# Kernel tuning notes

Measured on AMD Instinct MI355X. Metric: run time of the kernel, lower is better.

Reference implementation:

```python
import jax, jax.numpy as jnp
import numpy as np

D_MODEL, D_CTX, D_HEAD = 1024, 768, 16

def setup_inputs() -> dict:
    key = jax.random.key(0)
    ks = jax.random.split(key, 10)
    B, M, N = 8, 4096, 4096
    s = lambda d: 1.0 / np.sqrt(d)
    return {
        "x": jax.random.normal(ks[0], (B, M, D_MODEL), dtype=jnp.float32),
        "context": jax.random.normal(ks[1], (B, N, D_CTX), dtype=jnp.float32),
        "Wq": jax.random.uniform(ks[2], (D_MODEL, D_HEAD), jnp.float32, -s(D_MODEL), s(D_MODEL)),
        "bq": jax.random.uniform(ks[3], (D_HEAD,), jnp.float32, -s(D_MODEL), s(D_MODEL)),
        "Wk": jax.random.uniform(ks[4], (D_CTX, D_HEAD), jnp.float32, -s(D_CTX), s(D_CTX)),
        "bk": jax.random.uniform(ks[5], (D_HEAD,), jnp.float32, -s(D_CTX), s(D_CTX)),
        "Wv": jax.random.uniform(ks[6], (D_CTX, D_HEAD), jnp.float32, -s(D_CTX), s(D_CTX)),
        "bv": jax.random.uniform(ks[7], (D_HEAD,), jnp.float32, -s(D_CTX), s(D_CTX)),
        "Wo": jax.random.uniform(ks[8], (D_HEAD, D_MODEL), jnp.float32, -s(D_HEAD), s(D_HEAD)),
        "bo": jax.random.uniform(ks[9], (D_MODEL,), jnp.float32, -s(D_HEAD), s(D_HEAD)),
    }

def _kernel(t):
    # ELU+1 feature map (non-negative)
    return jax.nn.elu(t) + 1.0

def reference(x, context, Wq, bq, Wk, bk, Wv, bv, Wo, bo):
    Q = _kernel(x @ Wq + bq)            # (B, M, d_head)
    K = _kernel(context @ Wk + bk)      # (B, N, d_head)
    V = context @ Wv + bv               # (B, N, d_head)
    KtV = jnp.einsum('bnd,bne->bde', K, V)   # (B, d_head, d_head)
    num = jnp.einsum('bmd,bde->bme', Q, KtV) # (B, M, d_head)
    K_sum = K.sum(axis=1)                    # (B, d_head)
    denom = jnp.einsum('bmd,bd->bm', Q, K_sum)[..., None] + 1e-6
    out = num / denom                        # (B, M, d_head)
    return out @ Wo + bo                     # (B, M, d_model)
```

## Files before the change

kernel.cpp:

```cpp
#include <hip/hip_runtime.h>
#include <math.h>

#define B_   8
#define M_   4096
#define N_   4096
#define DM   1024
#define DC   768
#define DH   16
#define PD   8
#define KVBLOCKS (B_*N_/32)
#define QBLOCKS  (B_*M_/32)

typedef float v4f __attribute__((ext_vector_type(4)));
typedef __attribute__((ext_vector_type(8))) short short8v;
typedef __attribute__((ext_vector_type(4))) float f32x4;
typedef __attribute__((ext_vector_type(4))) int int4v;

__device__ __forceinline__ float elu1(float t) {
    return t > 0.0f ? t + 1.0f : expf(t);
}
__device__ __forceinline__ float4 ld4(const float* p) { return *reinterpret_cast<const float4*>(p); }
__device__ __forceinline__ void  st4(float* p, float4 v) { *reinterpret_cast<float4*>(p) = v; }
__device__ __forceinline__ void  st4nt(float* p, float4 v) {
    v4f w; w.x = v.x; w.y = v.y; w.z = v.z; w.w = v.w;
    __builtin_nontemporal_store(w, reinterpret_cast<v4f*>(p));
}
__device__ __forceinline__ void fma4(float4& a, float s, float4 w) {
    a.x = fmaf(s, w.x, a.x); a.y = fmaf(s, w.y, a.y);
    a.z = fmaf(s, w.z, a.z); a.w = fmaf(s, w.w, a.w);
}
__device__ __forceinline__ short f2bf(float f) {
    unsigned u = __float_as_uint(f);
    unsigned r = 0x7FFFu + ((u >> 16) & 1u);
    return (short)((u + r) >> 16);
}
__device__ __forceinline__ unsigned cvtpk(float a, float b) {
    unsigned r;
    asm("v_cvt_pk_bf16_f32 %0, %1, %2" : "=v"(r) : "v"(a), "v"(b));
    return r;
}
__device__ __forceinline__ short8v mk_frag(const float4& a, const float4& b) {
    int4v iv;
    iv.x = (int)cvtpk(a.x, a.y);
    iv.y = (int)cvtpk(a.z, a.w);
    iv.z = (int)cvtpk(b.x, b.y);
    iv.w = (int)cvtpk(b.z, b.w);
    union { int4v i; short8v s; } u; u.i = iv;
    return u.s;
}

__global__ __launch_bounds__(256) void prep(
    const float* __restrict__ Wq, const float* __restrict__ Wk,
    const float* __restrict__ Wv,
    short* __restrict__ fq, short* __restrict__ fk, short* __restrict__ fv)
{
    const int id = blockIdx.x * 256 + threadIdx.x;
    if (id >= 80 * 64) return;
    const int l  = id & 63;
    const int kt = id >> 6;
    const float* W; short* dst; int ktl;
    if (kt < 32)      { W = Wq; dst = fq; ktl = kt; }
    else if (kt < 56) { W = Wk; dst = fk; ktl = kt - 32; }
    else              { W = Wv; dst = fv; ktl = kt - 56; }
    const int k0 = ktl * 32 + (l >> 4) * 8;
    const int d  = l & 15;
    short* o = dst + ((size_t)ktl * 64 + l) * 8;
    #pragma unroll
    for (int j = 0; j < 8; ++j)
        o[j] = f2bf(W[(size_t)(k0 + j) * DH + d]);
}

__global__ __launch_bounds__(256) void kvr(
    const float* __restrict__ ctx,
    const short* __restrict__ fk, const short* __restrict__ fv,
    const float* __restrict__ bk, const float* __restrict__ bv,
    float* __restrict__ comb)
{
    __shared__ struct {
        float ka[2][2][16][17];
        float va[2][2][16][17];
        float sk[32][17];
        float sv[32][17];
    } sh;

    const int t  = threadIdx.x;
    const int l  = t & 63;
    const int w  = t >> 6;
    const int rt = w & 1;
    const int kh = w >> 1;
    const int g4 = l >> 4;
    const int lr = l & 15;

    float4 pa[PD], pb[PD];
    const size_t row0 = (size_t)blockIdx.x * 32;
    const float* src = ctx + (row0 + rt*16 + lr) * DC + kh*384 + g4*8;
    f32x4 accK = {0,0,0,0}, accV = {0,0,0,0};

    #pragma unroll
    for (int i = 0; i < PD; ++i) {
        pa[i] = ld4(src + i*32);
        pb[i] = ld4(src + i*32 + 4);
    }
    #pragma unroll
    for (int kt = 0; kt < 12; ++kt) {
        const int st = kt & (PD-1);
        const short8v a = mk_frag(pa[st], pb[st]);
        if (kt + PD < 12) {
            pa[st] = ld4(src + (kt+PD)*32);
            pb[st] = ld4(src + (kt+PD)*32 + 4);
        }
        const int ktg = kh*12 + kt;
        const short8v bkf = *reinterpret_cast<const short8v*>(fk + ((size_t)ktg*64 + l)*8);
        const short8v bvf = *reinterpret_cast<const short8v*>(fv + ((size_t)ktg*64 + l)*8);
        accK = __builtin_amdgcn_mfma_f32_16x16x32_bf16(a, bkf, accK, 0, 0, 0);
        accV = __builtin_amdgcn_mfma_f32_16x16x32_bf16(a, bvf, accV, 0, 0, 0);
    }

    #pragma unroll
    for (int j = 0; j < 4; ++j) {
        sh.ka[rt][kh][g4*4 + j][lr] = accK[j];
        sh.va[rt][kh][g4*4 + j][lr] = accV[j];
    }
    __syncthreads();

    #pragma unroll
    for (int i = t; i < 512; i += 256) {
        const int r = i >> 4, c = i & 15;
        const int rr = r >> 4, wr = r & 15;
        const float kk = sh.ka[rr][0][wr][c] + sh.ka[rr][1][wr][c] + bk[c];
        const float vv = sh.va[rr][0][wr][c] + sh.va[rr][1][wr][c] + bv[c];
        sh.sk[r][c] = elu1(kk);
        sh.sv[r][c] = vv;
    }
    __syncthreads();

    const int d = t >> 4, e = t & 15;
    float acc = 0.f;
    #pragma unroll 16
    for (int n = 0; n < 32; ++n) acc += sh.sk[n][d] * sh.sv[n][e];
    float* p = comb + (size_t)(blockIdx.x >> 7) * 272;
    atomicAdd(&p[t], acc);
    if (t < DH) {
        float ss = 0.f;
        #pragma unroll 16
        for (int n = 0; n < 32; ++n) ss += sh.sk[n][t];
        atomicAdd(&p[256 + t], ss);
    }
}

__global__ __launch_bounds__(256) void qproj(
    const float* __restrict__ x,
    const short* __restrict__ fq, const float* __restrict__ bq,
    const float* __restrict__ comb,
    const float* __restrict__ Wo, const float* __restrict__ bo,
    float* __restrict__ out)
{
    __shared__ float qa[2][2][16][17];
    __shared__ float ql[32 * DH];
    __shared__ float ol[32 * DH];
    __shared__ float kts[272];

    const int t  = threadIdx.x;
    const int l  = t & 63;
    const int w  = t >> 6;
    const int rt = w & 1;
    const int kh = w >> 1;
    const int g4 = l >> 4;
    const int lr = l & 15;
    const size_t row0 = (size_t)blockIdx.x * 32;
    const int b = blockIdx.x >> 7;

    const float* src = x + (row0 + rt*16 + lr) * DM + kh*512 + g4*8;
    float4 pa[PD], pb[PD];
    #pragma unroll
    for (int i = 0; i < PD; ++i) {
        pa[i] = ld4(src + i*32);
        pb[i] = ld4(src + i*32 + 4);
    }
    if (t < 68) st4(&kts[t*4], ld4(comb + (size_t)b*272 + t*4));

    f32x4 accQ = {0,0,0,0};
    #pragma unroll
    for (int kt = 0; kt < 16; ++kt) {
        const int st = kt & (PD-1);
        const short8v a = mk_frag(pa[st], pb[st]);
        if (kt + PD < 16) {
            pa[st] = ld4(src + (kt+PD)*32);
            pb[st] = ld4(src + (kt+PD)*32 + 4);
        }
        const int ktg = kh*16 + kt;
        const short8v bqf = *reinterpret_cast<const short8v*>(fq + ((size_t)ktg*64 + l)*8);
        accQ = __builtin_amdgcn_mfma_f32_16x16x32_bf16(a, bqf, accQ, 0, 0, 0);
    }
    #pragma unroll
    for (int j = 0; j < 4; ++j)
        qa[rt][kh][g4*4 + j][lr] = accQ[j];
    __syncthreads();

    #pragma unroll
    for (int i = t; i < 512; i += 256) {
        const int r = i >> 4, c = i & 15;
        const int rr = r >> 4, wr = r & 15;
        const float v = qa[rr][0][wr][c] + qa[rr][1][wr][c] + bq[c];
        ql[r*DH + c] = elu1(v);
    }
    __syncthreads();

    if (t < 128) {
        const float* qrow = &ql[(t >> 2) * DH];
        const int jj = (t & 3) * 4;
        float den = 1e-6f;
        float4 num = make_float4(0,0,0,0);
        #pragma unroll
        for (int d4 = 0; d4 < 4; ++d4) {
            const float4 q4  = ld4(&qrow[d4*4]);
            const float4 ks4 = ld4(&kts[256 + d4*4]);
            den += q4.x*ks4.x + q4.y*ks4.y + q4.z*ks4.z + q4.w*ks4.w;
            fma4(num, q4.x, ld4(&kts[(d4*4+0)*DH + jj]));
            fma4(num, q4.y, ld4(&kts[(d4*4+1)*DH + jj]));
            fma4(num, q4.z, ld4(&kts[(d4*4+2)*DH + jj]));
            fma4(num, q4.w, ld4(&kts[(d4*4+3)*DH + jj]));
        }
        const float inv = 1.0f / den;
        float4 o4; o4.x = num.x*inv; o4.y = num.y*inv; o4.z = num.z*inv; o4.w = num.w*inv;
        st4(&ol[(t >> 2)*DH + jj], o4);
    }
    __syncthreads();

    float4 wreg[16];
    #pragma unroll
    for (int e = 0; e < 16; ++e) wreg[e] = ld4(Wo + (size_t)e*DM + t*4);
    const float4 bov = ld4(bo + t*4);

    #pragma unroll 4
    for (int r = 0; r < 32; ++r) {
        float4 a = bov;
        #pragma unroll
        for (int eo = 0; eo < 4; ++eo) {
            const float4 o4 = ld4(&ol[r*DH + eo*4]);
            fma4(a, o4.x, wreg[eo*4+0]); fma4(a, o4.y, wreg[eo*4+1]);
            fma4(a, o4.z, wreg[eo*4+2]); fma4(a, o4.w, wreg[eo*4+3]);
        }
        st4nt(out + (row0 + r)*DM + t*4, a);
    }
}

extern "C" void kernel_launch(void* const* d_in, const int* in_sizes, int n_in,
                              void* d_out, int out_size, void* d_ws, size_t ws_size,
                              hipStream_t stream) {
    const float* x    = (const float*)d_in[0];
    const float* ctx  = (const float*)d_in[1];
    const float* Wq   = (const float*)d_in[2];
    const float* bq   = (const float*)d_in[3];
    const float* Wk   = (const float*)d_in[4];
    const float* bk   = (const float*)d_in[5];
    const float* Wv   = (const float*)d_in[6];
    const float* bv   = (const float*)d_in[7];
    const float* Wo   = (const float*)d_in[8];
    const float* bo   = (const float*)d_in[9];
    float* out = (float*)d_out;

    float* ws = (float*)d_ws;
    float* comb = ws;
    short* fq = (short*)(comb + (size_t)B_*272);
    short* fk = fq + (size_t)32*64*8;
    short* fv = fk + (size_t)24*64*8;

    hipMemsetAsync(comb, 0, (size_t)B_*272*sizeof(float), stream);
    prep<<<dim3(20), dim3(256), 0, stream>>>(Wq, Wk, Wv, fq, fk, fv);
    kvr<<<dim3(KVBLOCKS), dim3(256), 0, stream>>>(ctx, fk, fv, bk, bv, comb);
    qproj<<<dim3(QBLOCKS), dim3(256), 0, stream>>>(x, fq, bq, comb, Wo, bo, out);
}
```

Baseline: 74.72 us.

## Replace float atomics with per-block partials and last-block reduction

Each kvr block now writes its 272-float partial (KtV and K_sum) to a workspace slot instead of atomically adding into the per-batch accumulator. A per-batch counter, zeroed in prep, picks the last-finishing block, which sums the 128 partials into comb. This removes the hipMemsetAsync launch and the contention on 272 float atomics per batch from 128 blocks each. In exchange it adds partial-buffer traffic and a serial 128-way reduction in one block per batch, and the summation order becomes deterministic.

```diff
diff --git a/kernel.cpp b/kernel.cpp
--- a/kernel.cpp
+++ b/kernel.cpp
@@ -52,8 +52,10 @@
 __global__ __launch_bounds__(256) void prep(
     const float* __restrict__ Wq, const float* __restrict__ Wk,
     const float* __restrict__ Wv,
-    short* __restrict__ fq, short* __restrict__ fk, short* __restrict__ fv)
+    short* __restrict__ fq, short* __restrict__ fk, short* __restrict__ fv,
+    unsigned* __restrict__ cnt)
 {
+    if (blockIdx.x == 0 && threadIdx.x < B_) cnt[threadIdx.x] = 0;
     const int id = blockIdx.x * 256 + threadIdx.x;
     if (id >= 80 * 64) return;
     const int l  = id & 63;
@@ -74,7 +76,8 @@
     const float* __restrict__ ctx,
     const short* __restrict__ fk, const short* __restrict__ fv,
     const float* __restrict__ bk, const float* __restrict__ bv,
-    float* __restrict__ comb)
+    float* __restrict__ part, float* __restrict__ comb,
+    unsigned* __restrict__ cnt)
 {
     __shared__ struct {
         float ka[2][2][16][17];
@@ -82,6 +85,7 @@
         float sk[32][17];
         float sv[32][17];
     } sh;
+    __shared__ int is_last;
 
     const int t  = threadIdx.x;
     const int l  = t & 63;
@@ -138,13 +142,30 @@
     float acc = 0.f;
     #pragma unroll 16
     for (int n = 0; n < 32; ++n) acc += sh.sk[n][d] * sh.sv[n][e];
-    float* p = comb + (size_t)(blockIdx.x >> 7) * 272;
-    atomicAdd(&p[t], acc);
+    float* p = part + (size_t)blockIdx.x * 272;
+    p[t] = acc;
     if (t < DH) {
         float ss = 0.f;
         #pragma unroll 16
         for (int n = 0; n < 32; ++n) ss += sh.sk[n][t];
-        atomicAdd(&p[256 + t], ss);
+        p[256 + t] = ss;
+    }
+
+    const int b = blockIdx.x >> 7;
+    __threadfence();
+    if (t == 0) {
+        const unsigned old = atomicAdd(&cnt[b], 1u);
+        is_last = (old == 127u);
+    }
+    __syncthreads();
+    if (is_last) {
+        for (int idx = t; idx < 272; idx += 256) {
+            float s = 0.f;
+            #pragma unroll 8
+            for (int ch = 0; ch < 128; ++ch)
+                s += part[((size_t)b*128 + ch) * 272 + idx];
+            comb[(size_t)b*272 + idx] = s;
+        }
     }
 }
 
@@ -262,12 +283,13 @@
 
     float* ws = (float*)d_ws;
     float* comb = ws;
-    short* fq = (short*)(comb + (size_t)B_*272);
+    float* part = comb + (size_t)B_*272;
+    unsigned* cnt = (unsigned*)(part + (size_t)KVBLOCKS*272);
+    short* fq = (short*)(cnt + 64);
     short* fk = fq + (size_t)32*64*8;
     short* fv = fk + (size_t)24*64*8;
 
-    hipMemsetAsync(comb, 0, (size_t)B_*272*sizeof(float), stream);
-    prep<<<dim3(20), dim3(256), 0, stream>>>(Wq, Wk, Wv, fq, fk, fv);
-    kvr<<<dim3(KVBLOCKS), dim3(256), 0, stream>>>(ctx, fk, fv, bk, bv, comb);
+    prep<<<dim3(20), dim3(256), 0, stream>>>(Wq, Wk, Wv, fq, fk, fv, cnt);
+    kvr<<<dim3(KVBLOCKS), dim3(256), 0, stream>>>(ctx, fk, fv, bk, bv, part, comb, cnt);
     qproj<<<dim3(QBLOCKS), dim3(256), 0, stream>>>(x, fq, bq, comb, Wo, bo, out);
 }
```

After: 169.7 us. 2.27x slower.
